# Kernel tuning notes

Hardware: AMD Instinct MI355X
Metric: run time of the kernel (lower is better)

Reference implementation:

```python
import jax, jax.numpy as jnp
import numpy as np
import math

B, H4, W4, C = 4, 96, 312, 384
MAX_DISP = 48
ENT_T = 0.1
ENT_THR = 0.6
WIN_HALF = 12
BETA = 1.0
EPS = 1e-8
ROI = (0.2, 0.7, 2.0 / 3.0, 1.0)  # u0,u1,v0,v1 fractions


def _roi_mask():
    u0, u1, v0, v1 = ROI
    u0i = max(0, min(W4 - 1, int(math.floor(u0 * W4))))
    u1i = max(0, min(W4 - 1, int(math.ceil(u1 * W4)) - 1))
    v0i = max(0, min(H4 - 1, int(math.floor(v0 * H4))))
    v1i = max(0, min(H4 - 1, int(math.ceil(v1 * H4)) - 1))
    ys = jnp.arange(H4)[:, None]
    xs = jnp.arange(W4)[None, :]
    return (ys >= v0i) & (ys <= v1i) & (xs >= u0i) & (xs <= u1i)


def build_cost_volume(featL, featR):
    # featL/featR: [H4,W4,C] -> cost [D+1,H4,W4]; cost[d,:,x] = featL[:,x].featR[:,x-d], -inf for x<d
    xs = jnp.arange(W4)[None, :]
    def step(Rsh, d):
        s = jnp.einsum('hwc,hwc->hw', featL, Rsh)
        s = jnp.where(xs >= d, s, -jnp.inf)
        return jnp.roll(Rsh, 1, axis=1), s
    _, cost = jax.lax.scan(step, featR, jnp.arange(MAX_DISP + 1))
    return cost


def build_entropy_map(cv, T=ENT_T):
    m = jnp.max(cv, axis=0, keepdims=True)
    logits = (cv - m) / max(T, EPS)
    prob = jax.nn.softmax(logits, axis=0)
    p = jnp.maximum(prob, EPS)
    ent = -jnp.sum(p * jnp.log(p), axis=0)
    valid = jnp.isfinite(cv)
    Deff = jnp.maximum(jnp.sum(valid, axis=0), 1).astype(p.dtype)
    ent = jnp.where(Deff > 1, ent / (jnp.log(Deff) + EPS), jnp.zeros_like(ent))
    return jnp.clip(ent, 0.0, 1.0)


def invalid_run_extents(ent, thr):
    valid = ent <= thr
    x = jnp.broadcast_to(jnp.arange(W4)[None, :], (H4, W4))
    prev_valid = jax.lax.cummax(jnp.where(valid, x, -1), axis=1)
    prev_rev = jnp.flip(jax.lax.cummax(jnp.where(jnp.flip(valid, axis=1), x, -1), axis=1), axis=1)
    next_valid = jnp.where(prev_rev >= 0, W4 - 1 - prev_rev, W4)
    L = jnp.maximum(x - prev_valid - 1, 0)
    R = jnp.maximum(next_valid - x - 1, 0)
    a = jnp.maximum(x - L, 0)
    b = jnp.minimum(x + R, W4 - 1)
    return a, b, ~valid


def refine_cost(cv, ent_before, roi):
    Dp1 = MAX_DISP + 1
    a, b, invalid = invalid_run_extents(ent_before, ENT_THR)
    refine_mask = roi & invalid
    x = jnp.broadcast_to(jnp.arange(W4)[None, :], (H4, W4))
    a = jnp.maximum(a, jnp.maximum(x - WIN_HALF, 0))
    b = jnp.minimum(b, jnp.minimum(x + WIN_HALF, W4 - 1))
    finite = jnp.isfinite(cv)
    cvz = jnp.where(finite, cv, 0.0)
    pref = jnp.pad(jnp.cumsum(cvz, axis=2), ((0, 0), (0, 0), (1, 0)))
    cnt = jnp.pad(jnp.cumsum(finite.astype(cv.dtype), axis=2), ((0, 0), (0, 0), (1, 0)))
    a_idx = jnp.broadcast_to(a[None], (Dp1, H4, W4))
    b_idx = jnp.broadcast_to((b + 1)[None], (Dp1, H4, W4))
    num = jnp.take_along_axis(pref, b_idx, axis=2) - jnp.take_along_axis(pref, a_idx, axis=2)
    den = jnp.take_along_axis(cnt, b_idx, axis=2) - jnp.take_along_axis(cnt, a_idx, axis=2)
    agg = num / jnp.maximum(den, 1.0)
    agg = jnp.where(den > 0, agg, -jnp.inf)
    cv_ref = jnp.where(refine_mask[None], agg, cv)
    return cv_ref, build_entropy_map(cv_ref), refine_mask


def _per_sample_loss(featL, featR, student, roi):
    featL = jax.lax.stop_gradient(featL)  # stop_teacher_grad=True
    featR = jax.lax.stop_gradient(featR)
    E0 = build_cost_volume(featL, featR)
    ent0 = build_entropy_map(E0)
    E1, ent1, rm1 = refine_cost(E0, ent0, roi)
    E2, ent2, rm2 = refine_cost(E1, ent1, roi)  # two_stage=True
    base_cell = jnp.argmax(E0, axis=0).astype(jnp.float32)
    teacher_cell = jnp.argmax(E2, axis=0).astype(jnp.float32)  # teacher_type='arg'
    disp_filled = jnp.where(rm2, teacher_cell, base_cell)
    student_cell = student / 4.0  # student_unit='px'
    diff = student_cell - jax.lax.stop_gradient(disp_filled)
    ad = jnp.abs(diff)
    sl1 = jnp.where(ad < BETA, 0.5 * ad * ad / BETA, ad - 0.5 * BETA)
    mask = rm2.astype(jnp.float32)  # supervise_area='filled'
    return jnp.sum(sl1 * mask) / jnp.maximum(jnp.sum(mask), 1.0)


def setup_inputs() -> dict:
    key = jax.random.key(0)
    k1, k2, k3 = jax.random.split(key, 3)
    fL = jax.random.normal(k1, (B, H4, W4, C), dtype=jnp.float32)
    fR = jax.random.normal(k2, (B, H4, W4, C), dtype=jnp.float32)
    # features are L2-normalized per the module contract
    fL = fL / jnp.linalg.norm(fL, axis=-1, keepdims=True)
    fR = fR / jnp.linalg.norm(fR, axis=-1, keepdims=True)
    student = jax.random.uniform(k3, (B, H4, W4), dtype=jnp.float32) * (4.0 * MAX_DISP)
    return {"featL": fL, "featR": fR, "student_disp": student}


def reference(featL, featR, student_disp):
    roi = _roi_mask()
    losses = jax.vmap(lambda l, r, s: _per_sample_loss(l, r, s, roi))(featL, featR, student_disp)
    return jnp.mean(losses)
```

## Files before the change

kernel.cpp:

```cpp
#include <hip/hip_runtime.h>
#include <math.h>

#define BN 4
#define HN 96
#define WN 312
#define CN 384
#define D1 49

#define HROI0 64
#define HROI 32
#define XOFF 48
#define XLEN 192
#define CVSZ (BN*D1*HROI*XLEN)

#define TXC 64
#define KCC 16
#define RSTRIDE 116
#define NT (CN/KCC)

__global__ __launch_bounds__(64)
void k_cost(const float* __restrict__ Lf, const float* __restrict__ Rf, float* __restrict__ cv)
{
    __shared__ float Rs[2][KCC * RSTRIDE];
    const int t = threadIdx.x;
    const int xg = t & 15;
    const int dg = t >> 4;
    const int x0 = XOFF + blockIdx.x * TXC;
    const int hp = blockIdx.y;
    const int h = HROI0 + hp;
    const int b = blockIdx.z;
    const float* Lrow = Lf + (size_t)(b * HN + h) * WN * CN;
    const float* Rrow = Rf + (size_t)(b * HN + h) * WN * CN;
    const float* Rbase = Rrow + (size_t)(x0 - 48) * CN;
    const int rb = 4 * xg - 12 * dg + 36;
    const int d0 = 12 * dg;
    const int xbase = x0 + 4 * xg;

    const int srow[7] = { (t) >> 2, (t+64) >> 2, (t+128) >> 2, (t+192) >> 2,
                          (t+256) >> 2, (t+320) >> 2, (t+384) >> 2 };
    const int scq = t & 3;

    float acc[13][4];
#pragma unroll
    for (int j = 0; j < 13; j++)
#pragma unroll
        for (int i = 0; i < 4; i++) acc[j][i] = 0.f;

    {
        float4 rq[7];
#pragma unroll
        for (int ii = 0; ii < 7; ii++)
            rq[ii] = *(const float4*)(Rbase + (size_t)srow[ii] * CN + scq * 4);
#pragma unroll
        for (int ii = 0; ii < 7; ii++) {
            Rs[0][(4 * scq + 0) * RSTRIDE + srow[ii]] = rq[ii].x;
            Rs[0][(4 * scq + 1) * RSTRIDE + srow[ii]] = rq[ii].y;
            Rs[0][(4 * scq + 2) * RSTRIDE + srow[ii]] = rq[ii].z;
            Rs[0][(4 * scq + 3) * RSTRIDE + srow[ii]] = rq[ii].w;
        }
        __syncthreads();
    }

    for (int tt = 0; tt < NT; tt++) {
        const int c0 = tt * KCC;
        const float* rsr = Rs[tt & 1];
        float* rsw = Rs[(tt + 1) & 1];
        const bool more = (tt + 1 < NT);

        float4 rq[7];
        if (more) {
#pragma unroll
            for (int ii = 0; ii < 7; ii++)
                rq[ii] = *(const float4*)(Rbase + (size_t)srow[ii] * CN + c0 + KCC + scq * 4);
        }

        float Lc[4][KCC];
#pragma unroll
        for (int i = 0; i < 4; i++) {
            const float4* src = (const float4*)(Lrow + (size_t)(xbase + i) * CN + c0);
#pragma unroll
            for (int g = 0; g < 4; g++) {
                float4 v = src[g];
                Lc[i][4 * g + 0] = v.x;
                Lc[i][4 * g + 1] = v.y;
                Lc[i][4 * g + 2] = v.z;
                Lc[i][4 * g + 3] = v.w;
            }
        }

#pragma unroll
        for (int c = 0; c < KCC; c++) {
            const float4* rp4 = (const float4*)&rsr[c * RSTRIDE + rb];
            float4 q0 = rp4[0], q1 = rp4[1], q2 = rp4[2], q3 = rp4[3];
            float Rv[16] = {q0.x, q0.y, q0.z, q0.w, q1.x, q1.y, q1.z, q1.w,
                            q2.x, q2.y, q2.z, q2.w, q3.x, q3.y, q3.z, q3.w};
#pragma unroll
            for (int j = 0; j < 13; j++) {
#pragma unroll
                for (int i = 0; i < 4; i++)
                    acc[j][i] = fmaf(Lc[i][c], Rv[i - j + 12], acc[j][i]);
            }
        }

        if (more) {
#pragma unroll
            for (int ii = 0; ii < 7; ii++) {
                rsw[(4 * scq + 0) * RSTRIDE + srow[ii]] = rq[ii].x;
                rsw[(4 * scq + 1) * RSTRIDE + srow[ii]] = rq[ii].y;
                rsw[(4 * scq + 2) * RSTRIDE + srow[ii]] = rq[ii].z;
                rsw[(4 * scq + 3) * RSTRIDE + srow[ii]] = rq[ii].w;
            }
        }
        __syncthreads();
    }

    const int xl = xbase - XOFF;
#pragma unroll
    for (int j = 0; j < 13; j++) {
        int d = d0 + j;
        size_t base = ((size_t)(b * D1 + d) * HROI + hp) * XLEN + xl;
        *(float4*)(cv + base) = make_float4(acc[j][0], acc[j][1], acc[j][2], acc[j][3]);
    }
}

__device__ __forceinline__ float ent_from_lds(const float* E, int x)
{
    float v[D1];
#pragma unroll
    for (int d = 0; d < D1; d++) v[d] = E[d * XLEN + x];

    float m = v[0];
#pragma unroll
    for (int d = 1; d < D1; d++) m = fmaxf(m, v[d]);

    float S = 0.f;
    int cnt = 0;
#pragma unroll
    for (int d = 0; d < D1; d++) {
        if (isfinite(v[d])) cnt++;
        S += expf((v[d] - m) * 10.0f);
    }
    float lS = logf(S);
    float e_acc = 0.f;
#pragma unroll
    for (int d = 0; d < D1; d++) {
        float l = (v[d] - m) * 10.0f;
        float pe = expf(l) / S;
        if (pe > 1e-8f) e_acc -= pe * (l - lS);
        else            e_acc += 1.8420681e-7f;
    }
    float out = 0.f;
    if (cnt > 1) out = e_acc / (logf((float)cnt) + 1e-8f);
    return fminf(fmaxf(out, 0.f), 1.f);
}

__device__ __forceinline__ void extents3(const unsigned long long* vmask, int x,
                                         bool valid, int xglob,
                                         int* pa, int* pb, bool* prm)
{
    int prev = -1;
    int wi = x >> 6;
    unsigned long long m = vmask[wi] & (~0ULL >> (63 - (x & 63)));
    while (true) {
        if (m) { prev = (wi << 6) + 63 - __builtin_clzll(m); break; }
        if (--wi < 0) break;
        m = vmask[wi];
    }
    int nxt = XLEN;
    wi = x >> 6;
    m = vmask[wi] & (~0ULL << (x & 63));
    while (true) {
        if (m) { nxt = (wi << 6) + __builtin_ctzll(m); break; }
        if (++wi >= 3) break;
        m = vmask[wi];
    }
    int a = prev + 1;
    int lo = x - 12; if (lo < 0) lo = 0;
    if (a < lo) a = lo;
    int bb = (nxt > x) ? nxt - 1 : x;
    if (bb > XLEN - 1) bb = XLEN - 1;
    int hi = x + 12; if (hi > XLEN - 1) hi = XLEN - 1;
    if (bb > hi) bb = hi;
    *pa = a; *pb = bb;
    *prm = (!valid) && (xglob >= 62) && (xglob <= 218);
}

__global__ __launch_bounds__(192)
void k_post(const float* __restrict__ cv, const float* __restrict__ st,
            float* __restrict__ accum)
{
    __shared__ float E0[D1 * XLEN];
    __shared__ float E1[D1 * XLEN];
    __shared__ unsigned long long vmask[3];
    __shared__ float r1[3], r2[3];
    const int t = threadIdx.x;
    const int hp = blockIdx.x;
    const int b = blockIdx.y;
    const int xglob = XOFF + t;

#pragma unroll 7
    for (int d = 0; d < D1; d++)
        E0[d * XLEN + t] = cv[((size_t)(b * D1 + d) * HROI + hp) * XLEN + t];
    __syncthreads();

    bool valid = (ent_from_lds(E0, t) <= 0.6f);
    unsigned long long bal = __ballot(valid);
    if ((t & 63) == 0) vmask[t >> 6] = bal;
    __syncthreads();
    int a1, b1; bool rm1;
    extents3(vmask, t, valid, xglob, &a1, &b1, &rm1);

#pragma unroll 1
    for (int d = 0; d < D1; d++) {
        const float* row = &E0[d * XLEN];
        float val;
        if (rm1) {
            float num = 0.f;
#pragma unroll
            for (int k = 0; k < 25; k++) {
                int xx = a1 + k;
                if (xx <= b1) num += row[xx];
            }
            val = num / (float)(b1 - a1 + 1);
        } else {
            val = row[t];
        }
        E1[d * XLEN + t] = val;
    }
    __syncthreads();

    bool valid2 = (ent_from_lds(E1, t) <= 0.6f);
    unsigned long long bal2 = __ballot(valid2);
    if ((t & 63) == 0) vmask[t >> 6] = bal2;
    __syncthreads();
    int a2, b2; bool rm2;
    extents3(vmask, t, valid2, xglob, &a2, &b2, &rm2);

    float sl1 = 0.f, msk = 0.f;
    if (rm2) {
        float best = 0.f; int bi = 0;
#pragma unroll 1
        for (int d = 0; d < D1; d++) {
            const float* row = &E1[d * XLEN];
            float num = 0.f;
#pragma unroll
            for (int k = 0; k < 25; k++) {
                int xx = a2 + k;
                if (xx <= b2) num += row[xx];
            }
            float val = num / (float)(b2 - a2 + 1);
            if (d == 0 || val > best) { best = val; bi = d; }
        }
        float diff = st[((size_t)(b * HN + HROI0 + hp)) * WN + xglob] * 0.25f - (float)bi;
        float ad = fabsf(diff);
        sl1 = (ad < 1.f) ? 0.5f * ad * ad : ad - 0.5f;
        msk = 1.f;
    }
#pragma unroll
    for (int off = 32; off; off >>= 1) {
        sl1 += __shfl_down(sl1, off);
        msk += __shfl_down(msk, off);
    }
    if ((t & 63) == 0) { r1[t >> 6] = sl1; r2[t >> 6] = msk; }
    __syncthreads();
    if (t == 0) {
        float A = r1[0] + r1[1] + r1[2];
        float C = r2[0] + r2[1] + r2[2];
        atomicAdd(&accum[b * 2], A);
        atomicAdd(&accum[b * 2 + 1], C);
    }
}

__global__ void k_finalize(const float* __restrict__ accum, float* __restrict__ out)
{
    if (threadIdx.x == 0 && blockIdx.x == 0) {
        float s = 0.f;
        for (int b = 0; b < BN; b++) {
            float c = accum[2 * b + 1];
            if (c < 1.f) c = 1.f;
            s += accum[2 * b] / c;
        }
        out[0] = s * 0.25f;
    }
}

extern "C" void kernel_launch(void* const* d_in, const int* in_sizes, int n_in,
                              void* d_out, int out_size, void* d_ws, size_t ws_size,
                              hipStream_t stream)
{
    const float* fL = (const float*)d_in[0];
    const float* fR = (const float*)d_in[1];
    const float* st = (const float*)d_in[2];
    float* out = (float*)d_out;

    float* cv = (float*)d_ws;
    float* accum = cv + CVSZ;

    k_cost<<<dim3(3, HROI, BN), 64, 0, stream>>>(fL, fR, cv);
    hipMemsetAsync(accum, 0, 8 * sizeof(float), stream);
    k_post<<<dim3(HROI, BN), 192, 0, stream>>>(cv, st, accum);
    k_finalize<<<1, 64, 0, stream>>>(accum, out);
}
```

Measured before the change: 450.8 us.

## Fuse cost-volume and post-processing kernels; use prefix sums for window means

Merges the cost-volume kernel into the post-processing kernel, so each 192-thread block builds its row's cost volume directly in shared memory instead of writing it to global memory and reading it back. The feature loads are software-pipelined with two register sets and double-buffered LDS. The 25-tap window averages are replaced by per-disparity prefix sums, turning each window mean into one subtraction. The trade-off is fewer, larger blocks (128 blocks at one block per SM with heavy register use) in place of 384 small cost blocks, which reduces parallelism during the dominant dot-product phase.

```diff
diff --git a/kernel.cpp b/kernel.cpp
--- a/kernel.cpp
+++ b/kernel.cpp
@@ -11,123 +11,47 @@
 #define HROI 32
 #define XOFF 48
 #define XLEN 192
-#define CVSZ (BN*D1*HROI*XLEN)
-
+#define ESTR 193
 #define TXC 64
 #define KCC 16
 #define RSTRIDE 116
-#define NT (CN/KCC)
-
-__global__ __launch_bounds__(64)
-void k_cost(const float* __restrict__ Lf, const float* __restrict__ Rf, float* __restrict__ cv)
-{
-    __shared__ float Rs[2][KCC * RSTRIDE];
-    const int t = threadIdx.x;
-    const int xg = t & 15;
-    const int dg = t >> 4;
-    const int x0 = XOFF + blockIdx.x * TXC;
-    const int hp = blockIdx.y;
-    const int h = HROI0 + hp;
-    const int b = blockIdx.z;
-    const float* Lrow = Lf + (size_t)(b * HN + h) * WN * CN;
-    const float* Rrow = Rf + (size_t)(b * HN + h) * WN * CN;
-    const float* Rbase = Rrow + (size_t)(x0 - 48) * CN;
-    const int rb = 4 * xg - 12 * dg + 36;
-    const int d0 = 12 * dg;
-    const int xbase = x0 + 4 * xg;
-
-    const int srow[7] = { (t) >> 2, (t+64) >> 2, (t+128) >> 2, (t+192) >> 2,
-                          (t+256) >> 2, (t+320) >> 2, (t+384) >> 2 };
-    const int scq = t & 3;
-
-    float acc[13][4];
-#pragma unroll
-    for (int j = 0; j < 13; j++)
-#pragma unroll
-        for (int i = 0; i < 4; i++) acc[j][i] = 0.f;
-
-    {
-        float4 rq[7];
-#pragma unroll
-        for (int ii = 0; ii < 7; ii++)
-            rq[ii] = *(const float4*)(Rbase + (size_t)srow[ii] * CN + scq * 4);
-#pragma unroll
-        for (int ii = 0; ii < 7; ii++) {
-            Rs[0][(4 * scq + 0) * RSTRIDE + srow[ii]] = rq[ii].x;
-            Rs[0][(4 * scq + 1) * RSTRIDE + srow[ii]] = rq[ii].y;
-            Rs[0][(4 * scq + 2) * RSTRIDE + srow[ii]] = rq[ii].z;
-            Rs[0][(4 * scq + 3) * RSTRIDE + srow[ii]] = rq[ii].w;
-        }
-        __syncthreads();
-    }
-
-    for (int tt = 0; tt < NT; tt++) {
-        const int c0 = tt * KCC;
-        const float* rsr = Rs[tt & 1];
-        float* rsw = Rs[(tt + 1) & 1];
-        const bool more = (tt + 1 < NT);
-
-        float4 rq[7];
-        if (more) {
-#pragma unroll
-            for (int ii = 0; ii < 7; ii++)
-                rq[ii] = *(const float4*)(Rbase + (size_t)srow[ii] * CN + c0 + KCC + scq * 4);
-        }
-
-        float Lc[4][KCC];
-#pragma unroll
-        for (int i = 0; i < 4; i++) {
-            const float4* src = (const float4*)(Lrow + (size_t)(xbase + i) * CN + c0);
-#pragma unroll
-            for (int g = 0; g < 4; g++) {
-                float4 v = src[g];
-                Lc[i][4 * g + 0] = v.x;
-                Lc[i][4 * g + 1] = v.y;
-                Lc[i][4 * g + 2] = v.z;
-                Lc[i][4 * g + 3] = v.w;
-            }
-        }
-
-#pragma unroll
-        for (int c = 0; c < KCC; c++) {
-            const float4* rp4 = (const float4*)&rsr[c * RSTRIDE + rb];
-            float4 q0 = rp4[0], q1 = rp4[1], q2 = rp4[2], q3 = rp4[3];
-            float Rv[16] = {q0.x, q0.y, q0.z, q0.w, q1.x, q1.y, q1.z, q1.w,
-                            q2.x, q2.y, q2.z, q2.w, q3.x, q3.y, q3.z, q3.w};
-#pragma unroll
-            for (int j = 0; j < 13; j++) {
-#pragma unroll
-                for (int i = 0; i < 4; i++)
-                    acc[j][i] = fmaf(Lc[i][c], Rv[i - j + 12], acc[j][i]);
-            }
-        }
-
-        if (more) {
-#pragma unroll
-            for (int ii = 0; ii < 7; ii++) {
-                rsw[(4 * scq + 0) * RSTRIDE + srow[ii]] = rq[ii].x;
-                rsw[(4 * scq + 1) * RSTRIDE + srow[ii]] = rq[ii].y;
-                rsw[(4 * scq + 2) * RSTRIDE + srow[ii]] = rq[ii].z;
-                rsw[(4 * scq + 3) * RSTRIDE + srow[ii]] = rq[ii].w;
-            }
-        }
-        __syncthreads();
-    }
-
-    const int xl = xbase - XOFF;
-#pragma unroll
-    for (int j = 0; j < 13; j++) {
-        int d = d0 + j;
-        size_t base = ((size_t)(b * D1 + d) * HROI + hp) * XLEN + xl;
-        *(float4*)(cv + base) = make_float4(acc[j][0], acc[j][1], acc[j][2], acc[j][3]);
-    }
-}
-
-__device__ __forceinline__ float ent_from_lds(const float* E, int x)
+#define RST2 (KCC*RSTRIDE)
+
+#define LOADR(rq, c0) \
+    _Pragma("unroll") for (int ii = 0; ii < 7; ii++) \
+        rq[ii] = *(const float4*)(Rbase + (size_t)(sr0 + 16 * ii) * CN + (c0) + scq * 4);
+
+#define WRITER(Rsb, rq) \
+    _Pragma("unroll") for (int ii = 0; ii < 7; ii++) { \
+        const int row = sr0 + 16 * ii; \
+        (Rsb)[(4 * scq + 0) * RSTRIDE + row] = rq[ii].x; \
+        (Rsb)[(4 * scq + 1) * RSTRIDE + row] = rq[ii].y; \
+        (Rsb)[(4 * scq + 2) * RSTRIDE + row] = rq[ii].z; \
+        (Rsb)[(4 * scq + 3) * RSTRIDE + row] = rq[ii].w; }
+
+#define LOADL(Lc, c0) \
+    _Pragma("unroll") for (int i = 0; i < 4; i++) { \
+        const float4* src = (const float4*)(Lrow + (size_t)(xbase + i) * CN + (c0)); \
+        _Pragma("unroll") for (int g = 0; g < 4; g++) { \
+            float4 v = src[g]; \
+            Lc[i][4 * g + 0] = v.x; Lc[i][4 * g + 1] = v.y; \
+            Lc[i][4 * g + 2] = v.z; Lc[i][4 * g + 3] = v.w; } }
+
+#define COMPUTE(Lc, Rsb) \
+    _Pragma("unroll") for (int c = 0; c < KCC; c++) { \
+        const float4* rp4 = (const float4*)&(Rsb)[c * RSTRIDE + rb]; \
+        float4 q0 = rp4[0], q1 = rp4[1], q2 = rp4[2], q3 = rp4[3]; \
+        float Rv[16] = {q0.x, q0.y, q0.z, q0.w, q1.x, q1.y, q1.z, q1.w, \
+                        q2.x, q2.y, q2.z, q2.w, q3.x, q3.y, q3.z, q3.w}; \
+        _Pragma("unroll") for (int j = 0; j < 13; j++) \
+            _Pragma("unroll") for (int i = 0; i < 4; i++) \
+                acc[j][i] = fmaf(Lc[i][c], Rv[i - j + 12], acc[j][i]); }
+
+__device__ __forceinline__ float ent_col(const float* E, int x)
 {
     float v[D1];
 #pragma unroll
-    for (int d = 0; d < D1; d++) v[d] = E[d * XLEN + x];
+    for (int d = 0; d < D1; d++) v[d] = E[d * ESTR + x];
 
     float m = v[0];
 #pragma unroll
@@ -185,73 +109,129 @@
     *prm = (!valid) && (xglob >= 62) && (xglob <= 218);
 }
 
-__global__ __launch_bounds__(192)
-void k_post(const float* __restrict__ cv, const float* __restrict__ st,
-            float* __restrict__ accum)
-{
-    __shared__ float E0[D1 * XLEN];
-    __shared__ float E1[D1 * XLEN];
+__global__ __launch_bounds__(192, 1)
+void k_fused(const float* __restrict__ Lf, const float* __restrict__ Rf,
+             const float* __restrict__ st, float* __restrict__ accum)
+{
+    __shared__ float E0[D1 * ESTR];
+    __shared__ float Rpool[3 * 2 * RST2];
     __shared__ unsigned long long vmask[3];
     __shared__ float r1[3], r2[3];
+
     const int t = threadIdx.x;
+    const int w = t >> 6;
+    const int l = t & 63;
+    const int xg = l & 15;
+    const int dg = l >> 4;
     const int hp = blockIdx.x;
     const int b = blockIdx.y;
-    const int xglob = XOFF + t;
-
-#pragma unroll 7
-    for (int d = 0; d < D1; d++)
-        E0[d * XLEN + t] = cv[((size_t)(b * D1 + d) * HROI + hp) * XLEN + t];
-    __syncthreads();
-
-    bool valid = (ent_from_lds(E0, t) <= 0.6f);
+    const int h = HROI0 + hp;
+    const int x0 = XOFF + w * TXC;
+
+    const float* Lrow = Lf + (size_t)(b * HN + h) * WN * CN;
+    const float* Rbase = Rf + (size_t)(b * HN + h) * WN * CN + (size_t)(x0 - 48) * CN;
+    float* Rs0 = Rpool + w * 2 * RST2;
+    float* Rs1 = Rs0 + RST2;
+    const int rb = 4 * xg - 12 * dg + 36;
+    const int d0 = 12 * dg;
+    const int xbase = x0 + 4 * xg;
+    const int sr0 = l >> 2;
+    const int scq = l & 3;
+
+    float acc[13][4];
+#pragma unroll
+    for (int j = 0; j < 13; j++)
+#pragma unroll
+        for (int i = 0; i < 4; i++) acc[j][i] = 0.f;
+
+    float LcA[4][KCC], LcB[4][KCC];
+    float4 rqA[7], rqB[7];
+
+    LOADL(LcA, 0);
+    LOADR(rqA, 0);
+    WRITER(Rs0, rqA);
+    __syncthreads();
+    LOADR(rqB, KCC);
+    LOADL(LcB, KCC);
+
+#pragma unroll 1
+    for (int k = 0; k < 12; k++) {
+        const int c0 = k * 2 * KCC;
+        COMPUTE(LcA, Rs0);
+        WRITER(Rs1, rqB);
+        __syncthreads();
+        if (k < 11) { LOADR(rqA, c0 + 2 * KCC); LOADL(LcA, c0 + 2 * KCC); }
+        COMPUTE(LcB, Rs1);
+        if (k < 11) { WRITER(Rs0, rqA); }
+        __syncthreads();
+        if (k < 11) { LOADR(rqB, c0 + 3 * KCC); LOADL(LcB, c0 + 3 * KCC); }
+    }
+
+    {
+        const int xl = xbase - XOFF;
+#pragma unroll
+        for (int j = 0; j < 13; j++) {
+            float* er = &E0[(d0 + j) * ESTR + xl];
+            er[0] = acc[j][0]; er[1] = acc[j][1]; er[2] = acc[j][2]; er[3] = acc[j][3];
+        }
+    }
+    __syncthreads();
+
+    bool valid = (ent_col(E0, t) <= 0.6f);
     unsigned long long bal = __ballot(valid);
-    if ((t & 63) == 0) vmask[t >> 6] = bal;
+    if (l == 0) vmask[w] = bal;
     __syncthreads();
     int a1, b1; bool rm1;
-    extents3(vmask, t, valid, xglob, &a1, &b1, &rm1);
-
+    extents3(vmask, t, valid, XOFF + t, &a1, &b1, &rm1);
+
+    float* P = Rpool;
+    if (t < D1) {
+        const float* er = &E0[t * ESTR];
+        float* pr = &P[t * ESTR];
+        float s = 0.f;
+        pr[0] = 0.f;
+#pragma unroll 4
+        for (int x = 0; x < XLEN; x++) { s += er[x]; pr[x + 1] = s; }
+    }
+    __syncthreads();
+
+    if (rm1) {
+        const float den1 = (float)(b1 - a1 + 1);
 #pragma unroll 1
-    for (int d = 0; d < D1; d++) {
-        const float* row = &E0[d * XLEN];
-        float val;
-        if (rm1) {
-            float num = 0.f;
-#pragma unroll
-            for (int k = 0; k < 25; k++) {
-                int xx = a1 + k;
-                if (xx <= b1) num += row[xx];
-            }
-            val = num / (float)(b1 - a1 + 1);
-        } else {
-            val = row[t];
-        }
-        E1[d * XLEN + t] = val;
-    }
-    __syncthreads();
-
-    bool valid2 = (ent_from_lds(E1, t) <= 0.6f);
+        for (int d = 0; d < D1; d++) {
+            float num = P[d * ESTR + b1 + 1] - P[d * ESTR + a1];
+            E0[d * ESTR + t] = num / den1;
+        }
+    }
+    __syncthreads();
+
+    bool valid2 = (ent_col(E0, t) <= 0.6f);
     unsigned long long bal2 = __ballot(valid2);
-    if ((t & 63) == 0) vmask[t >> 6] = bal2;
+    if (l == 0) vmask[w] = bal2;
     __syncthreads();
     int a2, b2; bool rm2;
-    extents3(vmask, t, valid2, xglob, &a2, &b2, &rm2);
+    extents3(vmask, t, valid2, XOFF + t, &a2, &b2, &rm2);
+
+    if (t < D1) {
+        const float* er = &E0[t * ESTR];
+        float* pr = &P[t * ESTR];
+        float s = 0.f;
+        pr[0] = 0.f;
+#pragma unroll 4
+        for (int x = 0; x < XLEN; x++) { s += er[x]; pr[x + 1] = s; }
+    }
+    __syncthreads();
 
     float sl1 = 0.f, msk = 0.f;
     if (rm2) {
+        const float den2 = (float)(b2 - a2 + 1);
         float best = 0.f; int bi = 0;
 #pragma unroll 1
         for (int d = 0; d < D1; d++) {
-            const float* row = &E1[d * XLEN];
-            float num = 0.f;
-#pragma unroll
-            for (int k = 0; k < 25; k++) {
-                int xx = a2 + k;
-                if (xx <= b2) num += row[xx];
-            }
-            float val = num / (float)(b2 - a2 + 1);
+            float val = (P[d * ESTR + b2 + 1] - P[d * ESTR + a2]) / den2;
             if (d == 0 || val > best) { best = val; bi = d; }
         }
-        float diff = st[((size_t)(b * HN + HROI0 + hp)) * WN + xglob] * 0.25f - (float)bi;
+        float diff = st[(size_t)(b * HN + h) * WN + XOFF + t] * 0.25f - (float)bi;
         float ad = fabsf(diff);
         sl1 = (ad < 1.f) ? 0.5f * ad * ad : ad - 0.5f;
         msk = 1.f;
@@ -261,13 +241,11 @@
         sl1 += __shfl_down(sl1, off);
         msk += __shfl_down(msk, off);
     }
-    if ((t & 63) == 0) { r1[t >> 6] = sl1; r2[t >> 6] = msk; }
+    if (l == 0) { r1[w] = sl1; r2[w] = msk; }
     __syncthreads();
     if (t == 0) {
-        float A = r1[0] + r1[1] + r1[2];
-        float C = r2[0] + r2[1] + r2[2];
-        atomicAdd(&accum[b * 2], A);
-        atomicAdd(&accum[b * 2 + 1], C);
+        atomicAdd(&accum[b * 2], r1[0] + r1[1] + r1[2]);
+        atomicAdd(&accum[b * 2 + 1], r2[0] + r2[1] + r2[2]);
     }
 }
 
@@ -292,12 +270,9 @@
     const float* fR = (const float*)d_in[1];
     const float* st = (const float*)d_in[2];
     float* out = (float*)d_out;
-
-    float* cv = (float*)d_ws;
-    float* accum = cv + CVSZ;
-
-    k_cost<<<dim3(3, HROI, BN), 64, 0, stream>>>(fL, fR, cv);
+    float* accum = (float*)d_ws;
+
     hipMemsetAsync(accum, 0, 8 * sizeof(float), stream);
-    k_post<<<dim3(HROI, BN), 192, 0, stream>>>(cv, st, accum);
+    k_fused<<<dim3(HROI, BN), 192, 0, stream>>>(fL, fR, st, accum);
     k_finalize<<<1, 64, 0, stream>>>(accum, out);
 }
```

After: 736.9 us. 1.63x slower.
